# Optimization experiments

Measured on AMD Instinct MI355X. Metric: run time of the kernel, lower is better.

Reference implementation:

```python
import jax, jax.numpy as jnp
import numpy as np

K = 31          # local attention window (odd)
PAD = (K - 1) // 2
G = 8           # heads / groups
MC = 48         # model_complexity (attention out_features)
OF = 88         # output_features
BN_EPS = 1e-5


def conv2d(x, w, b):
    # x: [B,C,H,W], w: [O,I,3,3], 'SAME' == padding=1 for stride-1 3x3
    y = jax.lax.conv_general_dilated(x, w, (1, 1), 'SAME',
                                     dimension_numbers=('NCHW', 'OIHW', 'NCHW'))
    return y + b[None, :, None, None]


def bn(x, g, b, m, v):
    # inference-mode BatchNorm2d over channel dim of NCHW
    return (x - m[None, :, None, None]) * (g[None, :, None, None] /
           jnp.sqrt(v[None, :, None, None] + BN_EPS)) + b[None, :, None, None]


def maxpool_w2(x):
    # MaxPool2d((1,2)): pool width (freq) by 2
    return jax.lax.reduce_window(x, -jnp.inf, jax.lax.max,
                                 (1, 1, 1, 2), (1, 1, 1, 2), 'VALID')


def setup_inputs() -> dict:
    key = jax.random.key(0)
    ks = jax.random.split(key, 24)
    B, T, F = 8, 2560, 229
    C1, C2 = OF // 16, OF // 8          # 5, 11
    freq_feats = C2 * (F // 2 // 2)      # 11 * 57 = 627
    s = lambda k, shp, sc=0.05: jax.random.normal(k, shp, dtype=jnp.float32) * sc
    inp = {
        'spec':   jax.random.normal(ks[0], (B, T, F), dtype=jnp.float32),
        'c1_w': s(ks[1], (C1, 1, 3, 3)),  'c1_b': s(ks[2], (C1,)),
        'bn1_g': jnp.ones((C1,)), 'bn1_b': jnp.zeros((C1,)),
        'bn1_m': jnp.zeros((C1,)), 'bn1_v': jnp.ones((C1,)),
        'c2_w': s(ks[3], (C1, C1, 3, 3)), 'c2_b': s(ks[4], (C1,)),
        'bn2_g': jnp.ones((C1,)), 'bn2_b': jnp.zeros((C1,)),
        'bn2_m': jnp.zeros((C1,)), 'bn2_v': jnp.ones((C1,)),
        'c3_w': s(ks[5], (C2, C1, 3, 3)), 'c3_b': s(ks[6], (C2,)),
        'bn3_g': jnp.ones((C2,)), 'bn3_b': jnp.zeros((C2,)),
        'bn3_m': jnp.zeros((C2,)), 'bn3_v': jnp.ones((C2,)),
        'fc_w': s(ks[7], (OF, freq_feats)), 'fc_b': s(ks[8], (OF,)),
        'wq': s(ks[9], (MC, OF)), 'wk': s(ks[10], (MC, OF)), 'wv': s(ks[11], (MC, OF)),
        'rel': jax.random.normal(ks[12], (1, MC, K), dtype=jnp.float32),
        'ln_g': jnp.ones((MC,)), 'ln_b': jnp.zeros((MC,)),
        'lin_w': s(ks[13], (OF, MC)), 'lin_b': s(ks[14], (OF,)),
    }
    return inp


def reference(spec, c1_w, c1_b, bn1_g, bn1_b, bn1_m, bn1_v,
              c2_w, c2_b, bn2_g, bn2_b, bn2_m, bn2_v,
              c3_w, c3_b, bn3_g, bn3_b, bn3_m, bn3_v,
              fc_w, fc_b, wq, wk, wv, rel, ln_g, ln_b, lin_w, lin_b):
    B, T, F = spec.shape
    # ---- ConvStack (eval mode: BN uses running stats, dropout = identity) ----
    x = spec[:, None]                                  # [B,1,T,F]
    x = jax.nn.relu(bn(conv2d(x, c1_w, c1_b), bn1_g, bn1_b, bn1_m, bn1_v))
    x = jax.nn.relu(bn(conv2d(x, c2_w, c2_b), bn2_g, bn2_b, bn2_m, bn2_v))
    x = maxpool_w2(x)                                  # F -> F//2
    x = jax.nn.relu(bn(conv2d(x, c3_w, c3_b), bn3_g, bn3_b, bn3_m, bn3_v))
    x = maxpool_w2(x)                                  # F//2 -> F//4
    x = jnp.transpose(x, (0, 2, 1, 3)).reshape(B, T, -1)  # [B,T,C2*(F//4)]
    x = x @ fc_w.T + fc_b                              # [B,T,OF]

    # ---- MutliHeadAttention1D: local windowed attention via unfold ----
    q = x @ wq.T                                       # [B,T,MC]
    xp = jnp.pad(x, ((0, 0), (PAD, PAD), (0, 0)))
    k = xp @ wk.T                                      # [B,T+K-1,MC]
    v = xp @ wv.T
    idx = jnp.arange(T)[:, None] + jnp.arange(K)[None, :]   # [T,K]
    kw = jnp.transpose(k[:, idx], (0, 1, 3, 2)) + rel        # [B,T,MC,K]
    vw = jnp.transpose(v[:, idx], (0, 1, 3, 2))              # [B,T,MC,K]
    Dh = MC // G
    kw = kw.reshape(B, T, G, Dh, K)
    vw = vw.reshape(B, T, G, Dh, K)
    qh = q.reshape(B, T, G, Dh, 1)
    energy = (qh * kw).sum(-2, keepdims=True)          # [B,T,G,1,K]
    attn = jax.nn.softmax(energy, axis=-1)
    out = (attn * vw).sum(-1).reshape(B, T, MC)        # [B,T,MC]
    a = attn.squeeze(3)                                # [B,T,G,K]

    # ---- LayerNorm + Linear + sigmoid ----
    mu = out.mean(-1, keepdims=True)
    var = jnp.mean((out - mu) ** 2, axis=-1, keepdims=True)
    h = (out - mu) / jnp.sqrt(var + 1e-5) * ln_g + ln_b
    frame_pred = jax.nn.sigmoid(h @ lin_w.T + lin_b)   # [B,T,OF]
    return frame_pred, a
```

## Files before the change

### kernel.cpp

```cpp
#include <hip/hip_runtime.h>
#include <hip/hip_bf16.h>
#include <math.h>

#define B_    8
#define T_    2560
#define F_    229
#define C1_   5
#define C2_   11
#define W1_   114
#define W2_   57
#define KP_   640
#define OF_   88
#define MC_   48
#define G_    8
#define DH_   6
#define K_    31
#define PAD_  15
#define BN_EPS 1e-5f
#define LN_EPS 1e-5f
#define TS_   10
#define TT_   16

typedef __attribute__((ext_vector_type(8))) short short8;
typedef __attribute__((ext_vector_type(4))) float f32x4;
typedef _Float16 h2 __attribute__((ext_vector_type(2)));
typedef __fp16 fp16x2 __attribute__((ext_vector_type(2)));

static inline int cdiv(int a, int b) { return (a + b - 1) / b; }

union H2U { h2 h; unsigned u; };

__device__ inline h2 uph2(unsigned u) { H2U x; x.u = u; return x.h; }
__device__ inline unsigned packh2(float lo, float hi) {
    H2U x;
    x.h.x = (_Float16)lo;
    x.h.y = (_Float16)hi;
    return x.u;
}

#if __has_builtin(__builtin_amdgcn_cvt_pkrtz)
__device__ inline unsigned pkrtz(float a, float b) {
    union { fp16x2 v; unsigned u; } x;
    x.v = __builtin_amdgcn_cvt_pkrtz(a, b);
    return x.u;
}
#else
__device__ inline unsigned pkrtz(float a, float b) { return packh2(a, b); }
#endif

#if __has_builtin(__builtin_amdgcn_fdot2)
#define FDOT2(a, b, c) __builtin_amdgcn_fdot2((a), (b), (c), false)
#else
__device__ inline float FDOT2(h2 a, h2 b, float c) {
    return fmaf((float)a.x, (float)b.x, fmaf((float)a.y, (float)b.y, c));
}
#endif

__global__ __launch_bounds__(256) void wprime_kernel(const float* __restrict__ fc_w,
        const float* __restrict__ fc_b, const float* __restrict__ wq,
        const float* __restrict__ wk, const float* __restrict__ wv,
        __hip_bfloat16* __restrict__ wp, float* __restrict__ bp) {
    int idx = blockIdx.x * 256 + threadIdx.x;
    if (idx < 144 * KP_) {
        int o = idx / KP_;
        int kk = idx % KP_;
        const float* Wrow = (o < 48) ? (wq + o * 88)
                          : (o < 96) ? (wk + (o - 48) * 88) : (wv + (o - 96) * 88);
        float s = 0.f;
        if (kk < 627)
            for (int i = 0; i < 88; ++i) s = fmaf(Wrow[i], fc_w[(size_t)i * 627 + kk], s);
        wp[idx] = __float2bfloat16(s);
    } else if (idx < 144 * KP_ + 144) {
        int o = idx - 144 * KP_;
        const float* Wrow = (o < 48) ? (wq + o * 88)
                          : (o < 96) ? (wk + (o - 48) * 88) : (wv + (o - 96) * 88);
        float s = 0.f;
        for (int i = 0; i < 88; ++i) s = fmaf(Wrow[i], fc_b[i], s);
        bp[o] = s;
    }
}

__global__ __launch_bounds__(640, 8) void conv123_qkv_kernel(
        const float* __restrict__ spec,
        const float* __restrict__ c1w, const float* __restrict__ c1b,
        const float* __restrict__ g1, const float* __restrict__ b1,
        const float* __restrict__ m1, const float* __restrict__ v1,
        const float* __restrict__ c2w, const float* __restrict__ c2b,
        const float* __restrict__ g2, const float* __restrict__ b2,
        const float* __restrict__ m2, const float* __restrict__ v2,
        const float* __restrict__ c3w, const float* __restrict__ c3b,
        const float* __restrict__ g3, const float* __restrict__ b3,
        const float* __restrict__ m3, const float* __restrict__ v3,
        const __hip_bfloat16* __restrict__ Wp, const float* __restrict__ bp,
        float* __restrict__ Q) {
    __shared__ __align__(16) ushort x1t[70 * 240];
    __shared__ __align__(16) ushort x2u[7216];
    __shared__ __align__(16) unsigned w1p[60];
    __shared__ __align__(16) unsigned w2p[300];
    __shared__ __align__(16) unsigned w3p[660];
    __shared__ float scl1[5], shf1[5], scl2[5], shf2[5], scl3[11], shf3[11];
    int t0 = blockIdx.x * TS_;
    int b = blockIdx.y;
    int tid = threadIdx.x;

    if (tid < 15) {
        int co = tid / 3, dt = tid % 3;
        const float* wpt = c1w + co * 9 + dt * 3;
        unsigned* dst = &w1p[tid * 4];
        dst[0] = packh2(wpt[0], wpt[1]);
        dst[1] = packh2(wpt[2], 0.f);
        dst[2] = packh2(0.f, wpt[0]);
        dst[3] = packh2(wpt[1], wpt[2]);
    }
    for (int i = tid; i < 75; i += 640) {
        int r = i % 15;
        const float* wpt = c2w + (i / 15) * 45 + (r / 3) * 9 + (r % 3) * 3;
        unsigned* dst = &w2p[i * 4];
        dst[0] = packh2(wpt[0], wpt[1]);
        dst[1] = packh2(wpt[2], 0.f);
        dst[2] = packh2(0.f, wpt[0]);
        dst[3] = packh2(wpt[1], wpt[2]);
    }
    for (int i = tid; i < 165; i += 640) {
        int r = i % 15;
        const float* wpt = c3w + (i / 15) * 45 + (r / 3) * 9 + (r % 3) * 3;
        unsigned* dst = &w3p[i * 4];
        dst[0] = packh2(wpt[0], wpt[1]);
        dst[1] = packh2(wpt[2], 0.f);
        dst[2] = packh2(0.f, wpt[0]);
        dst[3] = packh2(wpt[1], wpt[2]);
    }
    if (tid < 5) {
        float s = g1[tid] * rsqrtf(v1[tid] + BN_EPS);
        scl1[tid] = s;
        shf1[tid] = (c1b[tid] - m1[tid]) * s + b1[tid];
    }
    if (tid >= 64 && tid < 69) {
        int c = tid - 64;
        float s = g2[c] * rsqrtf(v2[c] + BN_EPS);
        scl2[c] = s;
        shf2[c] = (c2b[c] - m2[c]) * s + b2[c];
    }
    if (tid >= 128 && tid < 139) {
        int c = tid - 128;
        float s = g3[c] * rsqrtf(v3[c] + BN_EPS);
        scl3[c] = s;
        shf3[c] = (c3b[c] - m3[c]) * s + b3[c];
    }
    {
        const float* sb = spec + (size_t)b * T_ * F_;
        for (int i = tid; i < 16 * 120; i += 640) {
            int row = i / 120;
            int pr = i - row * 120;
            int t = t0 - 3 + row;
            int c = 2 * pr - 4;
            float va = 0.f, vb = 0.f;
            if (t >= 0 && t < T_) {
                const float* rp = sb + (size_t)t * F_;
                if ((unsigned)c < 229u) va = rp[c];
                if ((unsigned)(c + 1) < 229u) vb = rp[c + 1];
            }
            *(unsigned*)&x2u[row * 240 + 2 * pr] = packh2(va, vb);
        }
        if (tid == 0) {
            uint4 z = {0u, 0u, 0u, 0u};
            *(uint4*)&x2u[7200] = z;
            *(uint4*)&x2u[7208] = z;
        }
    }
    __syncthreads();

    if (tid < 580) {
        int co = tid / 116;
        int rem = tid - co * 116;
        int q = rem >> 2;
        int rg = rem & 3;
        int rlo = rg * 3 + (rg ? 1 : 0);
        const unsigned* wb = &w1p[co * 12];
        uint4 wv0 = *(const uint4*)wb;
        uint4 wv1 = *(const uint4*)(wb + 4);
        uint4 wv2 = *(const uint4*)(wb + 8);
        h2 A1[3] = {uph2(wv0.x), uph2(wv1.x), uph2(wv2.x)};
        h2 B1[3] = {uph2(wv0.y), uph2(wv1.y), uph2(wv2.y)};
        h2 C1v[3] = {uph2(wv0.z), uph2(wv1.z), uph2(wv2.z)};
        h2 D1[3] = {uph2(wv0.w), uph2(wv1.w), uph2(wv2.w)};
        h2 X[6][5];
        const ushort* sp = x2u + 8 * q;
#pragma unroll
        for (int s = 0; s < 6; ++s) {
            const ushort* p = sp + (rlo + s) * 240;
            uint4 xq = *(const uint4*)p;
            unsigned xr = *(const unsigned*)(p + 8);
            X[s][0] = uph2(xq.x); X[s][1] = uph2(xq.y);
            X[s][2] = uph2(xq.z); X[s][3] = uph2(xq.w);
            X[s][4] = uph2(xr);
        }
        float s1 = scl1[co], h1 = shf1[co];
        int c0 = 8 * q - 3;
#pragma unroll
        for (int k = 0; k < 4; ++k) {
            int rr1 = rlo + k;
            int t = t0 - 2 + rr1;
            bool vt = (t >= 0 && t < T_);
            float y[8] = {0.f, 0.f, 0.f, 0.f, 0.f, 0.f, 0.f, 0.f};
#pragma unroll
            for (int dt = 0; dt < 3; ++dt) {
#pragma unroll
                for (int l = 0; l < 4; ++l) {
                    y[2 * l] = FDOT2(X[k + dt][l + 1], B1[dt],
                               FDOT2(X[k + dt][l], A1[dt], y[2 * l]));
                    y[2 * l + 1] = FDOT2(X[k + dt][l + 1], D1[dt],
                                   FDOT2(X[k + dt][l], C1v[dt], y[2 * l + 1]));
                }
            }
            unsigned pk[4];
#pragma unroll
            for (int m = 0; m < 4; ++m) {
                float ya = fmaxf(fmaf(y[2 * m], s1, h1), 0.f);
                float yb = fmaxf(fmaf(y[2 * m + 1], s1, h1), 0.f);
                ya = (vt && (c0 + 2 * m) >= 0) ? ya : 0.f;
                yb = (vt && (c0 + 2 * m + 1) >= 0) ? yb : 0.f;
                pk[m] = pkrtz(ya, yb);
            }
            uint4 pw = {pk[0], pk[1], pk[2], pk[3]};
            *(uint4*)&x1t[(rr1 * 5 + co) * 240 + 8 * q] = pw;
        }
    }
    if (tid < 70) {
        uint4 z = {0u, 0u, 0u, 0u};
        *(uint4*)&x1t[tid * 240 + 232] = z;
    }
    __syncthreads();

    float aE2[3][4], aO2[3][4];
    int co2 = 0, q22 = 0, rlo2 = 0;
    if (tid < 580) {
        co2 = tid / 116;
        int rem = tid - co2 * 116;
        q22 = rem >> 2;
        int rg = rem & 3;
        rlo2 = rg * 3;
#pragma unroll
        for (int i = 0; i < 3; ++i)
#pragma unroll
            for (int l = 0; l < 4; ++l) { aE2[i][l] = 0.f; aO2[i][l] = 0.f; }
        const ushort* px = x1t + 8 * q22;
        for (int ci = 0; ci < 5; ++ci) {
            const unsigned* wb = &w2p[(co2 * 5 + ci) * 12];
            uint4 wv0 = *(const uint4*)wb;
            uint4 wv1 = *(const uint4*)(wb + 4);
            uint4 wv2 = *(const uint4*)(wb + 8);
            h2 A[3] = {uph2(wv0.x), uph2(wv1.x), uph2(wv2.x)};
            h2 Bb[3] = {uph2(wv0.y), uph2(wv1.y), uph2(wv2.y)};
            h2 Cc[3] = {uph2(wv0.z), uph2(wv1.z), uph2(wv2.z)};
            h2 Dd[3] = {uph2(wv0.w), uph2(wv1.w), uph2(wv2.w)};
#pragma unroll
            for (int k = 0; k < 5; ++k) {
                const ushort* p = px + ((rlo2 + k) * 5 + ci) * 240;
                uint4 xq = *(const uint4*)p;
                unsigned xr = *(const unsigned*)(p + 8);
                h2 X[5] = {uph2(xq.x), uph2(xq.y), uph2(xq.z), uph2(xq.w), uph2(xr)};
#pragma unroll
                for (int dt = 0; dt < 3; ++dt) {
                    int lr = k - dt;
                    if (lr >= 0 && lr < 3) {
#pragma unroll
                        for (int l = 0; l < 4; ++l) {
                            aE2[lr][l] = FDOT2(X[l + 1], Bb[dt],
                                         FDOT2(X[l], A[dt], aE2[lr][l]));
                            aO2[lr][l] = FDOT2(X[l + 1], Dd[dt],
                                         FDOT2(X[l], Cc[dt], aO2[lr][l]));
                        }
                    }
                }
            }
        }
        float s = scl2[co2], sh = shf2[co2];
#pragma unroll
        for (int lr = 0; lr < 3; ++lr) {
            int r = rlo2 + lr;
            int t = t0 - 1 + r;
            bool vt = (t >= 0 && t < T_);
            float yv[4];
#pragma unroll
            for (int l = 0; l < 4; ++l) {
                int j = 4 * q22 - 1 + l;
                float y = fmaxf(fmaxf(fmaf(aE2[lr][l], s, sh), 0.f),
                                fmaxf(fmaf(aO2[lr][l], s, sh), 0.f));
                yv[l] = (vt && j >= 0 && j < 114) ? y : 0.f;
            }
            uint2 pw;
            pw.x = pkrtz(yv[0], yv[1]);
            pw.y = pkrtz(yv[2], yv[3]);
            *(uint2*)&x2u[(r * 5 + co2) * 120 + 4 * q22] = pw;
        }
    }
    __syncthreads();

    {
        uint4 z = {0u, 0u, 0u, 0u};
        uint4* x3t4 = (uint4*)x1t;
        x3t4[2 * tid] = z;
        x3t4[2 * tid + 1] = z;
    }
    __syncthreads();

    ushort* x3t = x1t;
    if (tid < 495) {
        int co = tid / 45;
        int rem = tid - co * 45;
        int pq = rem / 3;
        int rg = rem - pq * 3;
        int rlo = rg * 3;
        float aE[4][4], aO[4][4];
#pragma unroll
        for (int i = 0; i < 4; ++i)
#pragma unroll
            for (int l = 0; l < 4; ++l) { aE[i][l] = 0.f; aO[i][l] = 0.f; }
        const ushort* px = x2u + 8 * pq;
        for (int ci = 0; ci < 5; ++ci) {
            const unsigned* wb = &w3p[(co * 5 + ci) * 12];
            uint4 wv0 = *(const uint4*)wb;
            uint4 wv1 = *(const uint4*)(wb + 4);
            uint4 wv2 = *(const uint4*)(wb + 8);
            h2 A[3] = {uph2(wv0.x), uph2(wv1.x), uph2(wv2.x)};
            h2 Bb[3] = {uph2(wv0.y), uph2(wv1.y), uph2(wv2.y)};
            h2 Cc[3] = {uph2(wv0.z), uph2(wv1.z), uph2(wv2.z)};
            h2 Dd[3] = {uph2(wv0.w), uph2(wv1.w), uph2(wv2.w)};
#pragma unroll
            for (int k = 0; k < 6; ++k) {
                const ushort* p = px + ((rlo + k) * 5 + ci) * 120;
                uint4 xq = *(const uint4*)p;
                unsigned xr = *(const unsigned*)(p + 8);
                h2 X[5] = {uph2(xq.x), uph2(xq.y), uph2(xq.z), uph2(xq.w), uph2(xr)};
#pragma unroll
                for (int dt = 0; dt < 3; ++dt) {
                    int lr = k - dt;
                    if (lr >= 0 && lr < 4) {
#pragma unroll
                        for (int l = 0; l < 4; ++l) {
                            aE[lr][l] = FDOT2(X[l + 1], Bb[dt],
                                        FDOT2(X[l], A[dt], aE[lr][l]));
                            aO[lr][l] = FDOT2(X[l + 1], Dd[dt],
                                        FDOT2(X[l], Cc[dt], aO[lr][l]));
                        }
                    }
                }
            }
        }
        float s = scl3[co], sh = shf3[co];
#pragma unroll
        for (int lr = 0; lr < 4; ++lr) {
            int r = rlo + lr;
            int swz = (r & 7) << 4;
            char* rowb = (char*)x3t + r * 1280;
#pragma unroll
            for (int l = 0; l < 4; ++l) {
                int j = 4 * pq + l;
                if (j < 57) {
                    float y = fmaxf(fmaxf(fmaf(aE[lr][l], s, sh), 0.f),
                                    fmaxf(fmaf(aO[lr][l], s, sh), 0.f));
                    __hip_bfloat16 hv = __float2bfloat16(y);
                    int c = co * 57 + j;
                    *(ushort*)(rowb + ((c * 2) ^ swz)) = *(ushort*)&hv;
                }
            }
        }
    }
    __syncthreads();

    int w = tid >> 6;
    if (w < 9) {
        int lane = tid & 63;
        int r16 = lane & 15;
        int kq = (lane >> 4) * 8;
        const short* Ws = (const short*)Wp;
        const short* wrow = Ws + (size_t)(w * 16 + r16) * KP_ + kq;
        const char* x3b = (const char*)x3t + r16 * 1280;
        int swz = (r16 & 7) << 4;
        f32x4 acc = {0.f, 0.f, 0.f, 0.f};
#pragma unroll 4
        for (int kt = 0; kt < 20; ++kt) {
            int boff = ((kq + kt * 32) * 2) ^ swz;
            short8 a = *(const short8*)(x3b + boff);
            short8 bv = *(const short8*)(wrow + kt * 32);
            acc = __builtin_amdgcn_mfma_f32_16x16x32_bf16(a, bv, acc, 0, 0, 0);
        }
        int o = w * 16 + r16;
        float bias = bp[o];
        int rg4 = (lane >> 4) * 4;
#pragma unroll
        for (int i = 0; i < 4; ++i) {
            int r = rg4 + i;
            if (r < 10)
                Q[((size_t)b * T_ + t0 + r) * 144 + o] = acc[i] + bias;
        }
    }
}

__global__ __launch_bounds__(256) void attn_ln_kernel(const float* __restrict__ Q,
        const float* __restrict__ rel, const float* __restrict__ lng,
        const float* __restrict__ lnb, const float* __restrict__ lw,
        const float* __restrict__ lb, float* __restrict__ fp,
        float* __restrict__ aout) {
    __shared__ float smem[6088];
    __shared__ float mus[TT_], rss[TT_];
    float* kvt = smem;
    float* relT = smem + 4600;
    int b = blockIdx.y;
    int t0 = blockIdx.x * TT_;
    int tid = threadIdx.x;
    int h = tid & 1;
    int p = tid >> 1;
    int g = p & 7;
    int tl = p >> 3;
    for (int i = tid; i < 46 * 48; i += 256) {
        int row = i / 48, c2 = i % 48;
        int t = t0 - 15 + row;
        float2 v = {0.f, 0.f};
        if (t >= 0 && t < T_)
            v = *(const float2*)&Q[((size_t)b * T_ + t) * 144 + 48 + 2 * c2];
        *(float2*)&kvt[row * 100 + 2 * c2] = v;
    }
    for (int i = tid; i < 31 * 48; i += 256) {
        int kp = i / 48, j = i % 48;
        relT[i] = rel[j * 31 + kp];
    }
    const float* qg = &Q[((size_t)b * T_ + t0 + tl) * 144 + g * 6];
    float2 q01 = *(const float2*)qg;
    float2 q23 = *(const float2*)(qg + 2);
    float2 q45 = *(const float2*)(qg + 4);
    __syncthreads();
    float e[16];
    float m_h = -1e30f;
#pragma unroll
    for (int i = 0; i < 16; ++i) {
        int kp = 2 * i + h;
        if (kp < 31) {
            const float* kr = &kvt[(tl + kp) * 100 + g * 6];
            const float* rr = &relT[kp * 48 + g * 6];
            float2 k01 = *(const float2*)kr;
            float2 k23 = *(const float2*)(kr + 2);
            float2 k45 = *(const float2*)(kr + 4);
            float2 r01 = *(const float2*)rr;
            float2 r23 = *(const float2*)(rr + 2);
            float2 r45 = *(const float2*)(rr + 4);
            float s = fmaf(q01.x, k01.x + r01.x,
                      fmaf(q01.y, k01.y + r01.y,
                      fmaf(q23.x, k23.x + r23.x,
                      fmaf(q23.y, k23.y + r23.y,
                      fmaf(q45.x, k45.x + r45.x,
                           q45.y * (k45.y + r45.y))))));
            e[i] = s;
            m_h = fmaxf(m_h, s);
        }
    }
    float M = fmaxf(m_h, __shfl_xor(m_h, 1));
    float s_h = 0.f;
    float o0 = 0, o1 = 0, o2 = 0, o3 = 0, o4 = 0, o5 = 0;
#pragma unroll
    for (int i = 0; i < 16; ++i) {
        int kp = 2 * i + h;
        if (kp < 31) {
            float a = __expf(e[i] - M);
            e[i] = a;
            s_h += a;
            const float* vr = &kvt[(tl + kp) * 100 + 48 + g * 6];
            float2 v01 = *(const float2*)vr;
            float2 v23 = *(const float2*)(vr + 2);
            float2 v45 = *(const float2*)(vr + 4);
            o0 = fmaf(a, v01.x, o0); o1 = fmaf(a, v01.y, o1);
            o2 = fmaf(a, v23.x, o2); o3 = fmaf(a, v23.y, o3);
            o4 = fmaf(a, v45.x, o4); o5 = fmaf(a, v45.y, o5);
        }
    }
    float sum = s_h + __shfl_xor(s_h, 1);
    float inv = 1.f / sum;
    float t0s = o0 + __shfl_xor(o0, 1);
    float t1s = o1 + __shfl_xor(o1, 1);
    float t2s = o2 + __shfl_xor(o2, 1);
    float t3s = o3 + __shfl_xor(o3, 1);
    float t4s = o4 + __shfl_xor(o4, 1);
    float t5s = o5 + __shfl_xor(o5, 1);
    __syncthreads();
    float* abuf = smem;
    float* xr = smem + 3968;
#pragma unroll
    for (int i = 0; i < 16; ++i) {
        int kp = 2 * i + h;
        if (kp < 31) abuf[p * 31 + kp] = e[i] * inv;
    }
    if (h == 0) {
        float* xp = &xr[tl * 48 + g * 6];
        xp[0] = t0s * inv; xp[1] = t1s * inv; xp[2] = t2s * inv;
        xp[3] = t3s * inv; xp[4] = t4s * inv; xp[5] = t5s * inv;
    }
    __syncthreads();
    size_t base = ((size_t)b * T_ + t0) * 248;
    for (int i = tid; i < 992; i += 256) {
        float4 v = *(const float4*)&abuf[4 * i];
        *(float4*)&aout[base + 4 * i] = v;
    }
    if (tid < 64) {
        int r = tid >> 2, sub = tid & 3;
        const float* row = &xr[r * 48 + sub * 12];
        float s = 0.f;
#pragma unroll
        for (int c = 0; c < 12; ++c) s += row[c];
        s += __shfl_xor(s, 1);
        s += __shfl_xor(s, 2);
        float mu = s * (1.f / 48.f);
        float v2 = 0.f;
#pragma unroll
        for (int c = 0; c < 12; ++c) { float d = row[c] - mu; v2 = fmaf(d, d, v2); }
        v2 += __shfl_xor(v2, 1);
        v2 += __shfl_xor(v2, 2);
        if (sub == 0) {
            mus[r] = mu;
            rss[r] = rsqrtf(v2 * (1.f / 48.f) + LN_EPS);
        }
    }
    __syncthreads();
    for (int i = tid; i < TT_ * 48; i += 256) {
        int r = i / 48, c = i % 48;
        xr[i] = fmaf((xr[i] - mus[r]) * rss[r], lng[c], lnb[c]);
    }
    __syncthreads();
    size_t obase = ((size_t)b * T_ + t0) * 88;
    for (int i = tid; i < TT_ * 88; i += 256) {
        int o = i % 88, r = i / 88;
        const float* xp = &xr[r * 48];
        const float* wpp = &lw[o * 48];
        float s = lb[o];
#pragma unroll
        for (int c = 0; c < 48; c += 4) {
            float4 xv = *(const float4*)&xp[c];
            float4 wv = *(const float4*)&wpp[c];
            s = fmaf(xv.x, wv.x, s);
            s = fmaf(xv.y, wv.y, s);
            s = fmaf(xv.z, wv.z, s);
            s = fmaf(xv.w, wv.w, s);
        }
        fp[obase + i] = 1.f / (1.f + __expf(-s));
    }
}

extern "C" void kernel_launch(void* const* d_in, const int* in_sizes, int n_in,
                              void* d_out, int out_size, void* d_ws, size_t ws_size,
                              hipStream_t stream) {
    const float* spec = (const float*)d_in[0];
    const float* c1_w = (const float*)d_in[1];
    const float* c1_b = (const float*)d_in[2];
    const float* bn1_g = (const float*)d_in[3];
    const float* bn1_b = (const float*)d_in[4];
    const float* bn1_m = (const float*)d_in[5];
    const float* bn1_v = (const float*)d_in[6];
    const float* c2_w = (const float*)d_in[7];
    const float* c2_b = (const float*)d_in[8];
    const float* bn2_g = (const float*)d_in[9];
    const float* bn2_b = (const float*)d_in[10];
    const float* bn2_m = (const float*)d_in[11];
    const float* bn2_v = (const float*)d_in[12];
    const float* c3_w = (const float*)d_in[13];
    const float* c3_b = (const float*)d_in[14];
    const float* bn3_g = (const float*)d_in[15];
    const float* bn3_b = (const float*)d_in[16];
    const float* bn3_m = (const float*)d_in[17];
    const float* bn3_v = (const float*)d_in[18];
    const float* fc_w = (const float*)d_in[19];
    const float* fc_b = (const float*)d_in[20];
    const float* wq = (const float*)d_in[21];
    const float* wk = (const float*)d_in[22];
    const float* wv = (const float*)d_in[23];
    const float* rel = (const float*)d_in[24];
    const float* ln_g = (const float*)d_in[25];
    const float* ln_b = (const float*)d_in[26];
    const float* lin_w = (const float*)d_in[27];
    const float* lin_b = (const float*)d_in[28];

    float* ws = (float*)d_ws;
    __hip_bfloat16* wp_bf = (__hip_bfloat16*)(ws + 19000000);
    float* bp = ws + 19100000;
    float* Qb = ws + 23449600;

    float* frame_pred = (float*)d_out;
    float* a_out = frame_pred + (size_t)B_ * T_ * OF_;

    wprime_kernel<<<cdiv(144 * KP_ + 144, 256), 256, 0, stream>>>(fc_w, fc_b, wq, wk, wv,
                                                                  wp_bf, bp);
    conv123_qkv_kernel<<<dim3(T_ / TS_, B_), 640, 0, stream>>>(
        spec, c1_w, c1_b, bn1_g, bn1_b, bn1_m, bn1_v,
        c2_w, c2_b, bn2_g, bn2_b, bn2_m, bn2_v,
        c3_w, c3_b, bn3_g, bn3_b, bn3_m, bn3_v, wp_bf, bp, Qb);
    attn_ln_kernel<<<dim3(T_ / TT_, B_), 256, 0, stream>>>(Qb, rel, ln_g, ln_b, lin_w,
                                                           lin_b, frame_pred, a_out);
}
```

Baseline: 285.7 us.

## Enlarge attention tile, stage Q in LDS, fold x3 zeroing into idle threads

The attention kernel now handles 32 timesteps per block with 512 threads, loading Q, K and V rows together into shared memory as float4. Q is then read from LDS rather than fetched again from global memory, and the 30-row K/V halo is amortised over more outputs. In the conv kernel, the full zeroing pass and its barrier before conv3 are removed. Threads that are idle during conv3 now zero only the padding rows and the columns beyond 627. The trade-off is more LDS per block, which may reduce occupancy.

```diff
diff --git a/kernel.cpp b/kernel.cpp
--- a/kernel.cpp
+++ b/kernel.cpp
@@ -19,7 +19,7 @@
 #define BN_EPS 1e-5f
 #define LN_EPS 1e-5f
 #define TS_   10
-#define TT_   16
+#define TT_   32
 
 typedef __attribute__((ext_vector_type(8))) short short8;
 typedef __attribute__((ext_vector_type(4))) float f32x4;
@@ -232,14 +232,13 @@
     }
     __syncthreads();
 
-    float aE2[3][4], aO2[3][4];
-    int co2 = 0, q22 = 0, rlo2 = 0;
     if (tid < 580) {
-        co2 = tid / 116;
+        int co2 = tid / 116;
         int rem = tid - co2 * 116;
-        q22 = rem >> 2;
+        int q22 = rem >> 2;
         int rg = rem & 3;
-        rlo2 = rg * 3;
+        int rlo2 = rg * 3;
+        float aE2[3][4], aO2[3][4];
 #pragma unroll
         for (int i = 0; i < 3; ++i)
 #pragma unroll
@@ -297,14 +296,6 @@
     }
     __syncthreads();
 
-    {
-        uint4 z = {0u, 0u, 0u, 0u};
-        uint4* x3t4 = (uint4*)x1t;
-        x3t4[2 * tid] = z;
-        x3t4[2 * tid + 1] = z;
-    }
-    __syncthreads();
-
     ushort* x3t = x1t;
     if (tid < 495) {
         int co = tid / 45;
@@ -365,6 +356,20 @@
                     *(ushort*)(rowb + ((c * 2) ^ swz)) = *(ushort*)&hv;
                 }
             }
+        }
+    } else {
+        int idx = tid - 495;
+        uint4 z = {0u, 0u, 0u, 0u};
+        for (int i = idx; i < 480; i += 145) {
+            int row = 10 + i / 80;
+            int c16 = i - (i / 80) * 80;
+            *(uint4*)((char*)x3t + row * 1280 + c16 * 16) = z;
+        }
+        for (int i = idx; i < 130; i += 145) {
+            int r = i / 13;
+            int c = 627 + (i - r * 13);
+            int swz = (r & 7) << 4;
+            *(ushort*)((char*)x3t + r * 1280 + ((c * 2) ^ swz)) = 0;
         }
     }
     __syncthreads();
@@ -398,15 +403,15 @@
     }
 }
 
-__global__ __launch_bounds__(256) void attn_ln_kernel(const float* __restrict__ Q,
+__global__ __launch_bounds__(512) void attn_ln_kernel(const float* __restrict__ Q,
         const float* __restrict__ rel, const float* __restrict__ lng,
         const float* __restrict__ lnb, const float* __restrict__ lw,
         const float* __restrict__ lb, float* __restrict__ fp,
         float* __restrict__ aout) {
-    __shared__ float smem[6088];
+    __shared__ float smem[10664];
     __shared__ float mus[TT_], rss[TT_];
     float* kvt = smem;
-    float* relT = smem + 4600;
+    float* relT = smem + 9176;
     int b = blockIdx.y;
     int t0 = blockIdx.x * TT_;
     int tid = threadIdx.x;
@@ -414,30 +419,30 @@
     int p = tid >> 1;
     int g = p & 7;
     int tl = p >> 3;
-    for (int i = tid; i < 46 * 48; i += 256) {
-        int row = i / 48, c2 = i % 48;
+    for (int i = tid; i < 62 * 36; i += 512) {
+        int row = i / 36, c4 = i % 36;
         int t = t0 - 15 + row;
-        float2 v = {0.f, 0.f};
+        float4 v = {0.f, 0.f, 0.f, 0.f};
         if (t >= 0 && t < T_)
-            v = *(const float2*)&Q[((size_t)b * T_ + t) * 144 + 48 + 2 * c2];
-        *(float2*)&kvt[row * 100 + 2 * c2] = v;
-    }
-    for (int i = tid; i < 31 * 48; i += 256) {
+            v = *(const float4*)&Q[((size_t)b * T_ + t) * 144 + c4 * 4];
+        *(float4*)&kvt[row * 148 + c4 * 4] = v;
+    }
+    for (int i = tid; i < 31 * 48; i += 512) {
         int kp = i / 48, j = i % 48;
         relT[i] = rel[j * 31 + kp];
     }
-    const float* qg = &Q[((size_t)b * T_ + t0 + tl) * 144 + g * 6];
+    __syncthreads();
+    const float* qg = &kvt[(tl + 15) * 148 + g * 6];
     float2 q01 = *(const float2*)qg;
     float2 q23 = *(const float2*)(qg + 2);
     float2 q45 = *(const float2*)(qg + 4);
-    __syncthreads();
     float e[16];
     float m_h = -1e30f;
 #pragma unroll
     for (int i = 0; i < 16; ++i) {
         int kp = 2 * i + h;
         if (kp < 31) {
-            const float* kr = &kvt[(tl + kp) * 100 + g * 6];
+            const float* kr = &kvt[(tl + kp) * 148 + 48 + g * 6];
             const float* rr = &relT[kp * 48 + g * 6];
             float2 k01 = *(const float2*)kr;
             float2 k23 = *(const float2*)(kr + 2);
@@ -465,7 +470,7 @@
             float a = __expf(e[i] - M);
             e[i] = a;
             s_h += a;
-            const float* vr = &kvt[(tl + kp) * 100 + 48 + g * 6];
+            const float* vr = &kvt[(tl + kp) * 148 + 96 + g * 6];
             float2 v01 = *(const float2*)vr;
             float2 v23 = *(const float2*)(vr + 2);
             float2 v45 = *(const float2*)(vr + 4);
@@ -484,7 +489,7 @@
     float t5s = o5 + __shfl_xor(o5, 1);
     __syncthreads();
     float* abuf = smem;
-    float* xr = smem + 3968;
+    float* xr = smem + 7936;
 #pragma unroll
     for (int i = 0; i < 16; ++i) {
         int kp = 2 * i + h;
@@ -497,11 +502,11 @@
     }
     __syncthreads();
     size_t base = ((size_t)b * T_ + t0) * 248;
-    for (int i = tid; i < 992; i += 256) {
+    for (int i = tid; i < 1984; i += 512) {
         float4 v = *(const float4*)&abuf[4 * i];
         *(float4*)&aout[base + 4 * i] = v;
     }
-    if (tid < 64) {
+    if (tid < 128) {
         int r = tid >> 2, sub = tid & 3;
         const float* row = &xr[r * 48 + sub * 12];
         float s = 0.f;
@@ -521,13 +526,13 @@
         }
     }
     __syncthreads();
-    for (int i = tid; i < TT_ * 48; i += 256) {
+    for (int i = tid; i < TT_ * 48; i += 512) {
         int r = i / 48, c = i % 48;
         xr[i] = fmaf((xr[i] - mus[r]) * rss[r], lng[c], lnb[c]);
     }
     __syncthreads();
     size_t obase = ((size_t)b * T_ + t0) * 88;
-    for (int i = tid; i < TT_ * 88; i += 256) {
+    for (int i = tid; i < TT_ * 88; i += 512) {
         int o = i % 88, r = i / 88;
         const float* xp = &xr[r * 48];
         const float* wpp = &lw[o * 48];
@@ -592,6 +597,6 @@
         spec, c1_w, c1_b, bn1_g, bn1_b, bn1_m, bn1_v,
         c2_w, c2_b, bn2_g, bn2_b, bn2_m, bn2_v,
         c3_w, c3_b, bn3_g, bn3_b, bn3_m, bn3_v, wp_bf, bp, Qb);
-    attn_ln_kernel<<<dim3(T_ / TT_, B_), 256, 0, stream>>>(Qb, rel, ln_g, ln_b, lin_w,
+    attn_ln_kernel<<<dim3(T_ / TT_, B_), 512, 0, stream>>>(Qb, rel, ln_g, ln_b, lin_w,
                                                            lin_b, frame_pred, a_out);
 }
```

New measurement: 289.0 us. No clear change (+1.1%).
